# Performance work log

Measured on AMD Instinct MI355X. Metric: run time of the kernel, lower is better.

## Reference

```python
import jax, jax.numpy as jnp
import numpy as np

INPUTDIM = 256
OUTDIM = 256
GRIDSIZE = 300


def setup_inputs() -> dict:
    key = jax.random.key(0)
    k1, k2 = jax.random.split(key)
    x = jax.random.normal(k1, (1024, INPUTDIM), dtype=jnp.float32)
    scale = 1.0 / (np.sqrt(INPUTDIM) * np.sqrt(GRIDSIZE))
    fouriercoeffs = jax.random.normal(k2, (2, OUTDIM, INPUTDIM, GRIDSIZE), dtype=jnp.float32) * scale
    bias = jnp.zeros((1, OUTDIM), dtype=jnp.float32)
    return {"x": x, "fouriercoeffs": fouriercoeffs, "bias": bias}


def reference(x, fouriercoeffs, bias):
    # x: (B, I); fouriercoeffs: (2, O, I, G); bias: (1, O)
    outshape = x.shape[:-1] + (OUTDIM,)
    xf = x.reshape(-1, INPUTDIM)
    k = jnp.arange(1, GRIDSIZE + 1, dtype=xf.dtype)  # (G,)
    phase = xf[:, :, None] * k[None, None, :]        # (B, I, G)
    c = jnp.cos(phase)
    s = jnp.sin(phase)
    y = jnp.einsum('big,jig->bj', c, fouriercoeffs[0]) \
        + jnp.einsum('big,jig->bj', s, fouriercoeffs[1])
    y = y + bias
    return y.reshape(outshape)
```

## Files before the change

### kernel.cpp

```cpp
#include <hip/hip_runtime.h>

#define BATCH   1024
#define IDIM    256
#define ODIM    256
#define GRIDSZ  300
#define GP      304
#define KS_     64
#define IPW     4
#define CHUNKS  19
#define NSTEPS  (IPW*CHUNKS)
#define INV2PI  0.15915494309189535f

typedef __attribute__((ext_vector_type(8))) short  short8;
typedef __attribute__((ext_vector_type(4))) float  f32x4;
typedef __attribute__((ext_vector_type(4))) unsigned int u32x4;

__device__ __forceinline__ unsigned pk(float c, float s) {
  unsigned a = __float_as_uint(c) + 0x8000u;
  unsigned b = __float_as_uint(s) + 0x8000u;
  return __builtin_amdgcn_perm(b, a, 0x07060302u);
}

__device__ __forceinline__ void rot(float& c, float& s, float C, float S) {
  float t1 = s * S, t2 = c * S;
  float cn = __builtin_fmaf(c, C, -t1);
  s = __builtin_fmaf(s, C, t2);
  c = cn;
}

__device__ __forceinline__ void cossin(float rev, float& c, float& s) {
  c = __builtin_amdgcn_cosf(__builtin_amdgcn_fractf(rev));
  s = __builtin_amdgcn_cosf(__builtin_amdgcn_fractf(rev - 0.25f));
}

__global__ void init_out(const float* __restrict__ bias, float* __restrict__ out) {
  const int idx = blockIdx.x * 256 + threadIdx.x;
  out[idx] = bias[idx & (ODIM - 1)];
}

__global__ __launch_bounds__(256) void convertW(const float* __restrict__ fc,
                                                unsigned int* __restrict__ W) {
  const int qid = blockIdx.x * 256 + threadIdx.x;
  const int row = qid / 76;
  const int q   = qid - row * 76;
  u32x4 w = (u32x4){0u, 0u, 0u, 0u};
  if (q < 75) {
    const float* p0 = fc + (size_t)row * GRIDSZ + q * 4;
    const float* p1 = p0 + (size_t)ODIM * IDIM * GRIDSZ;
    const f32x4 a = *(const f32x4*)p0;
    const f32x4 b = *(const f32x4*)p1;
    w = (u32x4){pk(a.x, b.x), pk(a.y, b.y), pk(a.z, b.z), pk(a.w, b.w)};
  }
  *(u32x4*)(W + (size_t)row * GP + q * 4) = w;
}

__global__ __launch_bounds__(256, 4) void fkan2(
    const float* __restrict__ x, const unsigned int* __restrict__ W,
    float* __restrict__ out) {
  __shared__ alignas(16) unsigned int Blds[2][1024];

  const int tid = threadIdx.x, id = blockIdx.x;
  const int z = id & 7;
  const int m = (id >> 3) & 3;
  const int nk = (id >> 5) * 8 + z;
  const int n  = nk & 3;
  const int ks = nk >> 2;

  const int wave = tid >> 6, lane = tid & 63;
  const int fr = lane & 15, fq = lane >> 4;
  const int mbase = m * 256 + wave * 64;
  const int nbase = n * 64;

  f32x4 acc[4][4];
#pragma unroll
  for (int a_ = 0; a_ < 4; ++a_)
#pragma unroll
    for (int b_ = 0; b_ < 4; ++b_)
      acc[a_][b_] = (f32x4){0.f, 0.f, 0.f, 0.f};

  float r1c[4], r1s[4], r16c[4], r16s[4], sc_[4], ss_[4];

  int bo = ((nbase + wave * 16 + fr) * IDIM + ks * IPW) * GP + fq * 4;
  const int sa = wave * 256 + lane * 4;

  u32x4 bl = *(const u32x4*)(W + bo);
  *(u32x4*)&Blds[0][sa] = bl;

  int gs = 0, il = 0;

#pragma unroll 2
  for (int S = 0; S < NSTEPS; ++S) {
    __syncthreads();

    if (S < NSTEPS - 1) { bo += 16; bl = *(const u32x4*)(W + bo); }

    if (gs == 0) {
      const int i = ks * IPW + il;
#pragma unroll
      for (int tI = 0; tI < 4; ++tI) {
        const float xr = x[(size_t)(mbase + tI * 16 + fr) * IDIM + i] * INV2PI;
        cossin(xr, r1c[tI], r1s[tI]);
        cossin(16.0f * xr, r16c[tI], r16s[tI]);
        cossin((float)(fq * 4 + 1) * xr, sc_[tI], ss_[tI]);
      }
    }

    const unsigned int* buf = &Blds[S & 1][0];
    short8 bV0 = __builtin_bit_cast(short8, *(const u32x4*)(buf + lane * 4));
    short8 bV1 = __builtin_bit_cast(short8, *(const u32x4*)(buf + 256 + lane * 4));
    short8 bV2 = __builtin_bit_cast(short8, *(const u32x4*)(buf + 512 + lane * 4));
    short8 bV3 = __builtin_bit_cast(short8, *(const u32x4*)(buf + 768 + lane * 4));

#pragma unroll
    for (int tI = 0; tI < 4; ++tI) {
      float c = sc_[tI], s = ss_[tI];
      unsigned a0 = pk(c, s);
      rot(c, s, r1c[tI], r1s[tI]); unsigned a1 = pk(c, s);
      rot(c, s, r1c[tI], r1s[tI]); unsigned a2 = pk(c, s);
      rot(c, s, r1c[tI], r1s[tI]); unsigned a3 = pk(c, s);
      rot(sc_[tI], ss_[tI], r16c[tI], r16s[tI]);
      short8 aV = __builtin_bit_cast(short8, (u32x4){a0, a1, a2, a3});
      acc[tI][0] = __builtin_amdgcn_mfma_f32_16x16x32_bf16(aV, bV0, acc[tI][0], 0, 0, 0);
      acc[tI][1] = __builtin_amdgcn_mfma_f32_16x16x32_bf16(aV, bV1, acc[tI][1], 0, 0, 0);
      acc[tI][2] = __builtin_amdgcn_mfma_f32_16x16x32_bf16(aV, bV2, acc[tI][2], 0, 0, 0);
      acc[tI][3] = __builtin_amdgcn_mfma_f32_16x16x32_bf16(aV, bV3, acc[tI][3], 0, 0, 0);
    }

    if (S < NSTEPS - 1) *(u32x4*)&Blds[(S + 1) & 1][sa] = bl;

    gs++; if (gs == CHUNKS) { gs = 0; ++il; }
  }

  const int ob = mbase + fq * 4;
  const int oj = nbase + fr;
#pragma unroll
  for (int tI = 0; tI < 4; ++tI)
#pragma unroll
    for (int tJ = 0; tJ < 4; ++tJ) {
      float* dst = out + (size_t)(ob + tI * 16) * ODIM + (oj + tJ * 16);
#pragma unroll
      for (int rr = 0; rr < 4; ++rr)
        unsafeAtomicAdd(dst + rr * ODIM, acc[tI][tJ][rr]);
    }
}

__global__ __launch_bounds__(256, 3) void fkan_fb(
    const float* __restrict__ x, const float* __restrict__ fc,
    float* __restrict__ out) {
  const int tid = threadIdx.x, id = blockIdx.x;
  const int z = id & 7;
  const int m = (id >> 3) & 3;
  const int nk = (id >> 5) * 8 + z;
  const int n  = nk & 3;
  const int ks = nk >> 2;
  const int wave = tid >> 6, lane = tid & 63;
  const int fr = lane & 15, fq = lane >> 4;
  const int mbase = m * 256 + wave * 64;
  const int nbase = n * 64;

  f32x4 acc[4][4];
#pragma unroll
  for (int a_ = 0; a_ < 4; ++a_)
#pragma unroll
    for (int b_ = 0; b_ < 4; ++b_)
      acc[a_][b_] = (f32x4){0.f, 0.f, 0.f, 0.f};

  float r1c[4], r1s[4], r16c[4], r16s[4], sc_[4], ss_[4];
  f32x4 B0[4], B1[4];
  unsigned bF[4][4];
  int voff[4];
  const float* b1base = fc + (size_t)ODIM * IDIM * GRIDSZ;

#pragma unroll 1
  for (int il = 0; il < IPW; ++il) {
    const int i = ks * IPW + il;
#pragma unroll
    for (int tI = 0; tI < 4; ++tI) {
      float xr = x[(size_t)(mbase + tI * 16 + fr) * IDIM + i] * INV2PI;
      cossin(xr, r1c[tI], r1s[tI]);
      cossin(16.0f * xr, r16c[tI], r16s[tI]);
      cossin((float)(fq * 4 + 1) * xr, sc_[tI], ss_[tI]);
    }
#pragma unroll
    for (int tJ = 0; tJ < 4; ++tJ) {
      voff[tJ] = ((nbase + tJ * 16 + fr) * IDIM + i) * GRIDSZ + fq * 4;
      B0[tJ] = *(const f32x4*)(fc + voff[tJ]);
      B1[tJ] = *(const f32x4*)(b1base + voff[tJ]);
    }
#pragma unroll 1
    for (int chunk = 0; chunk < CHUNKS; ++chunk) {
#pragma unroll
      for (int tJ = 0; tJ < 4; ++tJ) {
        bF[tJ][0] = pk(B0[tJ].x, B1[tJ].x);
        bF[tJ][1] = pk(B0[tJ].y, B1[tJ].y);
        bF[tJ][2] = pk(B0[tJ].z, B1[tJ].z);
        bF[tJ][3] = pk(B0[tJ].w, B1[tJ].w);
      }
      if (chunk < CHUNKS - 1) {
        const int sub = ((chunk == CHUNKS - 2) & (fq == 3)) ? 4 : 0;
#pragma unroll
        for (int tJ = 0; tJ < 4; ++tJ) {
          voff[tJ] += 16;
          const int vu = voff[tJ] - sub;
          B0[tJ] = *(const f32x4*)(fc + vu);
          B1[tJ] = *(const f32x4*)(b1base + vu);
        }
      }
      if (chunk == CHUNKS - 1) {
        if (fq == 3) {
#pragma unroll
          for (int tI = 0; tI < 4; ++tI) { sc_[tI] = 0.0f; ss_[tI] = 0.0f; }
        }
      }
#pragma unroll
      for (int tI = 0; tI < 4; ++tI) {
        float c = sc_[tI], s = ss_[tI];
        unsigned a0 = pk(c, s);
        rot(c, s, r1c[tI], r1s[tI]); unsigned a1 = pk(c, s);
        rot(c, s, r1c[tI], r1s[tI]); unsigned a2 = pk(c, s);
        rot(c, s, r1c[tI], r1s[tI]); unsigned a3 = pk(c, s);
        rot(sc_[tI], ss_[tI], r16c[tI], r16s[tI]);
        short8 aV = __builtin_bit_cast(short8, (u32x4){a0, a1, a2, a3});
#pragma unroll
        for (int tJ = 0; tJ < 4; ++tJ) {
          short8 bV = __builtin_bit_cast(short8,
              (u32x4){bF[tJ][0], bF[tJ][1], bF[tJ][2], bF[tJ][3]});
          acc[tI][tJ] = __builtin_amdgcn_mfma_f32_16x16x32_bf16(aV, bV, acc[tI][tJ], 0, 0, 0);
        }
      }
    }
  }
  const int ob = mbase + fq * 4;
  const int oj = nbase + fr;
#pragma unroll
  for (int tI = 0; tI < 4; ++tI)
#pragma unroll
    for (int tJ = 0; tJ < 4; ++tJ) {
      float* dst = out + (size_t)(ob + tI * 16) * ODIM + (oj + tJ * 16);
#pragma unroll
      for (int rr = 0; rr < 4; ++rr)
        unsafeAtomicAdd(dst + rr * ODIM, acc[tI][tJ][rr]);
    }
}

extern "C" void kernel_launch(void* const* d_in, const int* in_sizes, int n_in,
                              void* d_out, int out_size, void* d_ws, size_t ws_size,
                              hipStream_t stream) {
  const float* x    = (const float*)d_in[0];
  const float* fc   = (const float*)d_in[1];
  const float* bias = (const float*)d_in[2];
  float* out = (float*)d_out;

  init_out<<<dim3(BATCH * ODIM / 256), dim3(256), 0, stream>>>(bias, out);

  const size_t need = (size_t)ODIM * IDIM * GP * 4;
  if (ws_size >= need) {
    unsigned int* W = (unsigned int*)d_ws;
    convertW<<<dim3(ODIM * IDIM * (GP / 4) / 256), dim3(256), 0, stream>>>(fc, W);
    fkan2<<<dim3(4 * 4 * KS_), dim3(256), 0, stream>>>(x, W, out);
  } else {
    fkan_fb<<<dim3(4 * 4 * KS_), dim3(256), 0, stream>>>(x, fc, out);
  }
}
```

Before: 363.2 us.

## Drop weight pre-conversion pass and read fp32 coefficients directly in main kernel

```diff
diff --git a/kernel.cpp b/kernel.cpp
--- a/kernel.cpp
+++ b/kernel.cpp
@@ -4,11 +4,9 @@
 #define IDIM    256
 #define ODIM    256
 #define GRIDSZ  300
-#define GP      304
 #define KS_     64
 #define IPW     4
 #define CHUNKS  19
-#define NSTEPS  (IPW*CHUNKS)
 #define INV2PI  0.15915494309189535f
 
 typedef __attribute__((ext_vector_type(8))) short  short8;
@@ -38,113 +36,7 @@
   out[idx] = bias[idx & (ODIM - 1)];
 }
 
-__global__ __launch_bounds__(256) void convertW(const float* __restrict__ fc,
-                                                unsigned int* __restrict__ W) {
-  const int qid = blockIdx.x * 256 + threadIdx.x;
-  const int row = qid / 76;
-  const int q   = qid - row * 76;
-  u32x4 w = (u32x4){0u, 0u, 0u, 0u};
-  if (q < 75) {
-    const float* p0 = fc + (size_t)row * GRIDSZ + q * 4;
-    const float* p1 = p0 + (size_t)ODIM * IDIM * GRIDSZ;
-    const f32x4 a = *(const f32x4*)p0;
-    const f32x4 b = *(const f32x4*)p1;
-    w = (u32x4){pk(a.x, b.x), pk(a.y, b.y), pk(a.z, b.z), pk(a.w, b.w)};
-  }
-  *(u32x4*)(W + (size_t)row * GP + q * 4) = w;
-}
-
-__global__ __launch_bounds__(256, 4) void fkan2(
-    const float* __restrict__ x, const unsigned int* __restrict__ W,
-    float* __restrict__ out) {
-  __shared__ alignas(16) unsigned int Blds[2][1024];
-
-  const int tid = threadIdx.x, id = blockIdx.x;
-  const int z = id & 7;
-  const int m = (id >> 3) & 3;
-  const int nk = (id >> 5) * 8 + z;
-  const int n  = nk & 3;
-  const int ks = nk >> 2;
-
-  const int wave = tid >> 6, lane = tid & 63;
-  const int fr = lane & 15, fq = lane >> 4;
-  const int mbase = m * 256 + wave * 64;
-  const int nbase = n * 64;
-
-  f32x4 acc[4][4];
-#pragma unroll
-  for (int a_ = 0; a_ < 4; ++a_)
-#pragma unroll
-    for (int b_ = 0; b_ < 4; ++b_)
-      acc[a_][b_] = (f32x4){0.f, 0.f, 0.f, 0.f};
-
-  float r1c[4], r1s[4], r16c[4], r16s[4], sc_[4], ss_[4];
-
-  int bo = ((nbase + wave * 16 + fr) * IDIM + ks * IPW) * GP + fq * 4;
-  const int sa = wave * 256 + lane * 4;
-
-  u32x4 bl = *(const u32x4*)(W + bo);
-  *(u32x4*)&Blds[0][sa] = bl;
-
-  int gs = 0, il = 0;
-
-#pragma unroll 2
-  for (int S = 0; S < NSTEPS; ++S) {
-    __syncthreads();
-
-    if (S < NSTEPS - 1) { bo += 16; bl = *(const u32x4*)(W + bo); }
-
-    if (gs == 0) {
-      const int i = ks * IPW + il;
-#pragma unroll
-      for (int tI = 0; tI < 4; ++tI) {
-        const float xr = x[(size_t)(mbase + tI * 16 + fr) * IDIM + i] * INV2PI;
-        cossin(xr, r1c[tI], r1s[tI]);
-        cossin(16.0f * xr, r16c[tI], r16s[tI]);
-        cossin((float)(fq * 4 + 1) * xr, sc_[tI], ss_[tI]);
-      }
-    }
-
-    const unsigned int* buf = &Blds[S & 1][0];
-    short8 bV0 = __builtin_bit_cast(short8, *(const u32x4*)(buf + lane * 4));
-    short8 bV1 = __builtin_bit_cast(short8, *(const u32x4*)(buf + 256 + lane * 4));
-    short8 bV2 = __builtin_bit_cast(short8, *(const u32x4*)(buf + 512 + lane * 4));
-    short8 bV3 = __builtin_bit_cast(short8, *(const u32x4*)(buf + 768 + lane * 4));
-
-#pragma unroll
-    for (int tI = 0; tI < 4; ++tI) {
-      float c = sc_[tI], s = ss_[tI];
-      unsigned a0 = pk(c, s);
-      rot(c, s, r1c[tI], r1s[tI]); unsigned a1 = pk(c, s);
-      rot(c, s, r1c[tI], r1s[tI]); unsigned a2 = pk(c, s);
-      rot(c, s, r1c[tI], r1s[tI]); unsigned a3 = pk(c, s);
-      rot(sc_[tI], ss_[tI], r16c[tI], r16s[tI]);
-      short8 aV = __builtin_bit_cast(short8, (u32x4){a0, a1, a2, a3});
-      acc[tI][0] = __builtin_amdgcn_mfma_f32_16x16x32_bf16(aV, bV0, acc[tI][0], 0, 0, 0);
-      acc[tI][1] = __builtin_amdgcn_mfma_f32_16x16x32_bf16(aV, bV1, acc[tI][1], 0, 0, 0);
-      acc[tI][2] = __builtin_amdgcn_mfma_f32_16x16x32_bf16(aV, bV2, acc[tI][2], 0, 0, 0);
-      acc[tI][3] = __builtin_amdgcn_mfma_f32_16x16x32_bf16(aV, bV3, acc[tI][3], 0, 0, 0);
-    }
-
-    if (S < NSTEPS - 1) *(u32x4*)&Blds[(S + 1) & 1][sa] = bl;
-
-    gs++; if (gs == CHUNKS) { gs = 0; ++il; }
-  }
-
-  const int ob = mbase + fq * 4;
-  const int oj = nbase + fr;
-#pragma unroll
-  for (int tI = 0; tI < 4; ++tI)
-#pragma unroll
-    for (int tJ = 0; tJ < 4; ++tJ) {
-      float* dst = out + (size_t)(ob + tI * 16) * ODIM + (oj + tJ * 16);
-#pragma unroll
-      for (int rr = 0; rr < 4; ++rr)
-        unsafeAtomicAdd(dst + rr * ODIM, acc[tI][tJ][rr]);
-    }
-}
-
-__global__ __launch_bounds__(256, 3) void fkan_fb(
+__global__ __launch_bounds__(256, 3) void fkan_main(
     const float* __restrict__ x, const float* __restrict__ fc,
     float* __restrict__ out) {
   const int tid = threadIdx.x, id = blockIdx.x;
@@ -230,6 +122,7 @@
       }
     }
   }
+
   const int ob = mbase + fq * 4;
   const int oj = nbase + fr;
 #pragma unroll
@@ -252,13 +145,5 @@
   float* out = (float*)d_out;
 
   init_out<<<dim3(BATCH * ODIM / 256), dim3(256), 0, stream>>>(bias, out);
-
-  const size_t need = (size_t)ODIM * IDIM * GP * 4;
-  if (ws_size >= need) {
-    unsigned int* W = (unsigned int*)d_ws;
-    convertW<<<dim3(ODIM * IDIM * (GP / 4) / 256), dim3(256), 0, stream>>>(fc, W);
-    fkan2<<<dim3(4 * 4 * KS_), dim3(256), 0, stream>>>(x, W, out);
-  } else {
-    fkan_fb<<<dim3(4 * 4 * KS_), dim3(256), 0, stream>>>(x, fc, out);
-  }
+  fkan_main<<<dim3(4 * 4 * KS_), dim3(256), 0, stream>>>(x, fc, out);
 }
```

Result: slower. 499.3 us (+37.5%).
